# Kernel optimization log

Measured on AMD Instinct MI355X. Metric: run time of the kernel, lower is better.

The kernel has to match this reference:

```python
import jax, jax.numpy as jnp
import numpy as np

N_EMBED = 384
N_HEAD = 6
HEAD_SIZE = N_EMBED // N_HEAD  # 64
LN_EPS = 1e-5


def setup_inputs() -> dict:
    key = jax.random.key(0)
    ks = jax.random.split(key, 12)
    B, T = 128, 256
    s_in = 1.0 / np.sqrt(N_EMBED)
    s_ff = 1.0 / np.sqrt(4 * N_EMBED)
    return {
        "x": jax.random.normal(ks[0], (B, T, N_EMBED), jnp.float32),
        "Wq": jax.random.normal(ks[1], (N_HEAD, N_EMBED, HEAD_SIZE), jnp.float32) * s_in,
        "Wk": jax.random.normal(ks[2], (N_HEAD, N_EMBED, HEAD_SIZE), jnp.float32) * s_in,
        "Wv": jax.random.normal(ks[3], (N_HEAD, N_EMBED, HEAD_SIZE), jnp.float32) * s_in,
        "Wproj": jax.random.normal(ks[4], (N_EMBED, N_EMBED), jnp.float32) * s_in,
        "bproj": jnp.zeros((N_EMBED,), jnp.float32),
        "W1": jax.random.normal(ks[5], (N_EMBED, 4 * N_EMBED), jnp.float32) * s_in,
        "b1": jnp.zeros((4 * N_EMBED,), jnp.float32),
        "W2": jax.random.normal(ks[6], (4 * N_EMBED, N_EMBED), jnp.float32) * s_ff,
        "b2": jnp.zeros((N_EMBED,), jnp.float32),
        "ln1_g": jnp.ones((N_EMBED,), jnp.float32),
        "ln1_b": jnp.zeros((N_EMBED,), jnp.float32),
        "ln2_g": jnp.ones((N_EMBED,), jnp.float32),
        "ln2_b": jnp.zeros((N_EMBED,), jnp.float32),
    }


def _layernorm(x, g, b):
    mu = jnp.mean(x, axis=-1, keepdims=True)
    var = jnp.mean(jnp.square(x - mu), axis=-1, keepdims=True)
    return (x - mu) * jax.lax.rsqrt(var + LN_EPS) * g + b


def _attention(xn, Wq, Wk, Wv, Wproj, bproj):
    B, T, C = xn.shape
    q = jnp.einsum("btc,hcd->bhtd", xn, Wq)
    k = jnp.einsum("btc,hcd->bhtd", xn, Wk)
    v = jnp.einsum("btc,hcd->bhtd", xn, Wv)
    # NOTE: original scales by C**-0.5 with C = n_embed (384), not head_size
    scores = jnp.einsum("bhtd,bhsd->bhts", q, k) * (C ** -0.5)
    causal = jnp.tril(jnp.ones((T, T), bool))
    scores = jnp.where(causal, scores, -jnp.inf)
    wei = jax.nn.softmax(scores, axis=-1)
    out = jnp.einsum("bhts,bhsd->bhtd", wei, v)
    out = out.transpose(0, 2, 1, 3).reshape(B, T, N_EMBED)  # concat heads
    return out @ Wproj + bproj


def reference(x, Wq, Wk, Wv, Wproj, bproj, W1, b1, W2, b2, ln1_g, ln1_b, ln2_g, ln2_b):
    x = x + _attention(_layernorm(x, ln1_g, ln1_b), Wq, Wk, Wv, Wproj, bproj)
    h = _layernorm(x, ln2_g, ln2_b)
    ff = jax.nn.relu(h @ W1 + b1) @ W2 + b2
    return x + ff
```

## Files before the change

kernel.cpp:

```cpp
#include <hip/hip_runtime.h>
#include <hip/hip_bf16.h>

typedef __hip_bfloat16 bf16;
typedef __attribute__((ext_vector_type(8))) short bf16x8;
typedef __attribute__((ext_vector_type(4))) float f32x4;

#define CEMB 384
#define NHEAD 6
#define HSZ 64
#define TSEQ 256
#define BATCH 128
#define MROWS (BATCH*TSEQ)
#define FDIM 1536
#define QSCALE 0.05103103630798288f
#define SMAX 8.0f

#define AS1 __attribute__((address_space(1)))
#define AS3 __attribute__((address_space(3)))
__device__ __forceinline__ void gload16(const void* g, void* l){
  __builtin_amdgcn_global_load_lds((const AS1 unsigned*)(g), (AS3 unsigned*)(l), 16, 0, 0);
}
__device__ __forceinline__ float b2f(unsigned short u){
  unsigned int xi = ((unsigned int)u)<<16; float f; __builtin_memcpy(&f,&xi,4); return f;
}

__global__ __launch_bounds__(256) void ln_kernel(const float* __restrict__ x,
    const float* __restrict__ gam, const float* __restrict__ bet,
    bf16* __restrict__ y)
{
  const int row  = blockIdx.x*4 + (threadIdx.x>>6);
  const int lane = threadIdx.x & 63;
  const float* xr = x + (size_t)row*CEMB;
  float v[6]; float s = 0.f;
  #pragma unroll
  for (int i=0;i<6;i++){ v[i] = xr[lane + i*64]; s += v[i]; }
  #pragma unroll
  for (int m=1;m<64;m<<=1) s += __shfl_xor(s, m, 64);
  const float mu = s * (1.0f/CEMB);
  float qs = 0.f;
  #pragma unroll
  for (int i=0;i<6;i++){ v[i] -= mu; qs += v[i]*v[i]; }
  #pragma unroll
  for (int m=1;m<64;m<<=1) qs += __shfl_xor(qs, m, 64);
  const float rs = rsqrtf(qs*(1.0f/CEMB) + 1e-5f);
  bf16* yr = y + (size_t)row*CEMB;
  #pragma unroll
  for (int i=0;i<6;i++){
    int c = lane + i*64;
    yr[c] = __float2bfloat16(v[i]*rs*gam[c] + bet[c]);
  }
}

__global__ __launch_bounds__(256) void ln_kernel_b(const bf16* __restrict__ x,
    const float* __restrict__ gam, const float* __restrict__ bet,
    bf16* __restrict__ y)
{
  const int row  = blockIdx.x*4 + (threadIdx.x>>6);
  const int lane = threadIdx.x & 63;
  const ushort2* xr = (const ushort2*)(x + (size_t)row*CEMB);
  float v[6]; float s = 0.f;
  #pragma unroll
  for (int i=0;i<3;i++){
    ushort2 u = xr[lane + i*64];
    v[2*i]   = b2f(u.x); v[2*i+1] = b2f(u.y);
    s += v[2*i] + v[2*i+1];
  }
  #pragma unroll
  for (int m=1;m<64;m<<=1) s += __shfl_xor(s, m, 64);
  const float mu = s * (1.0f/CEMB);
  float qs = 0.f;
  #pragma unroll
  for (int i=0;i<6;i++){ v[i] -= mu; qs += v[i]*v[i]; }
  #pragma unroll
  for (int m=1;m<64;m<<=1) qs += __shfl_xor(qs, m, 64);
  const float rs = rsqrtf(qs*(1.0f/CEMB) + 1e-5f);
  bf16* yr = y + (size_t)row*CEMB;
  #pragma unroll
  for (int i=0;i<3;i++)
    #pragma unroll
    for (int j=0;j<2;j++){
      int c = (lane + i*64)*2 + j;
      yr[c] = __float2bfloat16(v[2*i+j]*rs*gam[c] + bet[c]);
    }
}

__global__ __launch_bounds__(256) void transpose_to_bf16(const float* __restrict__ src,
    bf16* __restrict__ dst, int K, int N)
{
  __shared__ float tile[32][33];
  const int n0 = blockIdx.x*32, k0 = blockIdx.y*32;
  src += (size_t)blockIdx.z*K*N;
  dst += (size_t)blockIdx.z*K*N;
  const int c = threadIdx.x & 31, r8 = threadIdx.x >> 5;
  #pragma unroll
  for (int i=0;i<4;i++)
    tile[r8 + i*8][c] = src[(size_t)(k0 + r8 + i*8)*N + n0 + c];
  __syncthreads();
  #pragma unroll
  for (int i=0;i<4;i++)
    dst[(size_t)(n0 + r8 + i*8)*K + k0 + c] = __float2bfloat16(tile[c][r8 + i*8]);
}

__global__ __launch_bounds__(256) void transpose_qkv(const float* __restrict__ Wq,
    const float* __restrict__ Wk, const float* __restrict__ Wv, bf16* __restrict__ dst)
{
  __shared__ float tile[32][33];
  const int z = blockIdx.z;
  const float* src = (z < 6) ? Wq : (z < 12 ? Wk : Wv);
  src += (size_t)(z % 6) * CEMB * HSZ;
  dst += (size_t)z * CEMB * HSZ;
  const int n0 = blockIdx.x*32, k0 = blockIdx.y*32;
  const int c = threadIdx.x & 31, r8 = threadIdx.x >> 5;
  #pragma unroll
  for (int i=0;i<4;i++)
    tile[r8 + i*8][c] = src[(size_t)(k0 + r8 + i*8)*HSZ + n0 + c];
  __syncthreads();
  #pragma unroll
  for (int i=0;i<4;i++)
    dst[(size_t)(n0 + r8 + i*8)*CEMB + k0 + c] = __float2bfloat16(tile[c][r8 + i*8]);
}

template<int EPI, int NN, int NK>
__global__ __launch_bounds__(512) void gemm5(
    const bf16* __restrict__ A, const bf16* __restrict__ BT,
    const float* __restrict__ bias, const float* __restrict__ resid,
    float* __restrict__ outf, bf16* __restrict__ outb0,
    bf16* __restrict__ outb1, bf16* __restrict__ outb2)
{
  constexpr int K = NK*32;
  constexpr int N = NN*128;
  __shared__ char lA[3][256*64];
  __shared__ char lB[3][128*64];
  const int cpx = gridDim.x >> 3;
  const int wg  = (blockIdx.x & 7)*cpx + (blockIdx.x >> 3);
  const int bm = (wg / NN)*256, bn = (wg % NN)*128;
  const int t = threadIdx.x, lane = t & 63, wid = t >> 6;
  const int wr = (wid>>1)*64, wc = (wid&1)*64;
  const int g = lane >> 4, fr = lane & 15;
  const size_t rowK2 = (size_t)K*2;
  f32x4 acc[4][4] = {};

  auto stage = [&](int sl, int kt){
    const size_t ko = (size_t)kt*64;
    #pragma unroll
    for (int i=0;i<2;i++){
      int slot = t + i*512;
      int row = slot>>2, blk = slot&3;
      gload16((const char*)A + (size_t)(bm+row)*rowK2 + ko + ((blk ^ ((row>>1)&3))<<4),
              lA[sl] + slot*16);
    }
    {
      int row = t>>2, blk = t&3;
      gload16((const char*)BT + (size_t)(bn+row)*rowK2 + ko + ((blk ^ ((row>>1)&3))<<4),
              lB[sl] + t*16);
    }
  };

  stage(0,0); stage(1,1); stage(2,2);
  #pragma unroll 1
  for (int kt=0; kt<NK; ++kt){
    const int rem = NK-1-kt;
    if (rem >= 2)      asm volatile("s_waitcnt vmcnt(6)" ::: "memory");
    else if (rem == 1) asm volatile("s_waitcnt vmcnt(3)" ::: "memory");
    else               asm volatile("s_waitcnt vmcnt(0)" ::: "memory");
    __builtin_amdgcn_s_barrier();
    const int cur = kt%3;
    bf16x8 af[4], bq[4];
    #pragma unroll
    for (int mi=0;mi<4;mi++){
      int row = wr + mi*16 + fr;
      af[mi] = *(const bf16x8*)(lA[cur] + row*64 + ((g ^ ((row>>1)&3))<<4));
    }
    #pragma unroll
    for (int nj=0;nj<4;nj++){
      int row = wc + nj*16 + fr;
      bq[nj] = *(const bf16x8*)(lB[cur] + row*64 + ((g ^ ((row>>1)&3))<<4));
    }
    asm volatile("s_waitcnt lgkmcnt(0)" ::: "memory");
    __builtin_amdgcn_sched_barrier(0);
    __builtin_amdgcn_s_barrier();
    if (kt+3 < NK) stage(cur, kt+3);
    __builtin_amdgcn_s_setprio(1);
    #pragma unroll
    for (int mi=0;mi<4;mi++)
      #pragma unroll
      for (int nj=0;nj<4;nj++)
        acc[mi][nj] = __builtin_amdgcn_mfma_f32_16x16x32_bf16(af[mi], bq[nj], acc[mi][nj], 0, 0, 0);
    __builtin_amdgcn_s_setprio(0);
  }

  if constexpr (EPI==0){
    const int sel = bn/CEMB;
    bf16* dst = sel==0 ? outb0 : (sel==1 ? outb1 : outb2);
    const float sc = sel==0 ? QSCALE : 1.0f;
    const int nb = bn - sel*CEMB;
    #pragma unroll
    for (int nj=0;nj<4;nj++){
      const int nn = nb + wc + nj*16 + fr;
      const int hh = nn>>6, dd = nn&63;
      #pragma unroll
      for (int mi=0;mi<4;mi++){
        const int m0 = bm + wr + mi*16 + 4*g;
        const int bb = m0>>8, tt0 = m0&255;
        bf16* p = dst + ((size_t)(bb*NHEAD + hh)*TSEQ + tt0)*HSZ + dd;
        #pragma unroll
        for (int e=0;e<4;e++)
          p[(size_t)e*HSZ] = __float2bfloat16(acc[mi][nj][e]*sc);
      }
    }
  } else {
    #pragma unroll
    for (int mi=0;mi<4;mi++)
      #pragma unroll
      for (int nj=0;nj<4;nj++)
        #pragma unroll
        for (int e=0;e<4;e++){
          const int m = bm + wr + mi*16 + 4*g + e;
          const int n = bn + wc + nj*16 + fr;
          const float vacc = acc[mi][nj][e];
          if constexpr (EPI==1){
            outb0[(size_t)m*N + n] = __float2bfloat16(vacc + bias[n] + resid[(size_t)m*N + n]);
          } else {
            float z = vacc + bias[n];
            outb0[(size_t)m*N + n] = __float2bfloat16(z > 0.f ? z : 0.f);
          }
        }
  }
}

template<int NK>
__global__ __launch_bounds__(512, 2) void gemm8n(
    const bf16* __restrict__ A, const bf16* __restrict__ BT,
    const float* __restrict__ bias, const bf16* __restrict__ residb,
    float* __restrict__ outf)
{
  constexpr int K = NK*64;
  __shared__ char lds[114688];
  const int cpx = gridDim.x >> 3;
  const int wg  = (blockIdx.x & 7)*cpx + (blockIdx.x >> 3);
  const int bm = (wg >> 1)*256, bn = (wg & 1)*192;
  const int t = threadIdx.x, lane = t & 63, wid = t >> 6;
  const int wm = wid >> 2, wn = wid & 3;
  const int g = lane >> 4, fr = lane & 15;
  const size_t rowb = (size_t)K*2;
  const int sblkA = ((t&3) ^ ((t>>3)&3)) << 4;
  const int swzA  = (g ^ ((fr>>1)&3)) << 4;
  f32x4 acc[8][3] = {};

  const char* Ag = (const char*)A + (size_t)(bm + (t>>2))*rowb + sblkA;
  const size_t rstep = rowb*128;

  auto stgA = [&](int KH, int sl, int kt2){
    const char* src = Ag + (size_t)kt2*128 + KH*64;
    char* dst = lds + sl*32768 + KH*16384 + wid*1024;
    gload16(src,         dst);
    gload16(src + rstep, dst + 8192);
  };
  auto stgB = [&](int sl, int kt2){
    #pragma unroll
    for (int j=0;j<3;j++){
      int slot = t + j*512;
      int row = slot>>3, blk = slot&7;
      gload16((const char*)BT + (size_t)(bn + row)*rowb + (size_t)kt2*128 + ((blk ^ (row&7))<<4),
              lds + 65536 + sl*24576 + j*8192 + wid*1024);
    }
  };
  auto rdA = [&](bf16x8* af, int sl, int MH, int KS){
    const char* p = lds + sl*32768 + KS*16384 + (wm*128 + MH*64 + fr)*64 + swzA;
    #pragma unroll
    for (int mi=0;mi<4;mi++) af[mi] = *(const bf16x8*)(p + mi*1024);
  };
  auto rdB = [&](bf16x8* bq, int sl, int ks){
    #pragma unroll
    for (int nj=0;nj<3;nj++){
      int row = wn*48 + nj*16 + fr;
      bq[nj] = *(const bf16x8*)(lds + 65536 + sl*24576 + row*128 + (((ks*4+g) ^ (row&7))<<4));
    }
  };

#define MFMA12(MH) \
  __builtin_amdgcn_s_setprio(1); \
  _Pragma("unroll") \
  for (int mi=0;mi<4;mi++){ \
    _Pragma("unroll") \
    for (int nj=0;nj<3;nj++) \
      acc[(MH)*4+mi][nj] = __builtin_amdgcn_mfma_f32_16x16x32_bf16(af[mi], bq[nj], acc[(MH)*4+mi][nj], 0, 0, 0); \
  } \
  __builtin_amdgcn_s_setprio(0);

  stgA(0,0,0); stgB(0,0); stgA(1,0,0);
  asm volatile("s_waitcnt vmcnt(2)" ::: "memory");
  __builtin_amdgcn_s_barrier();

  #pragma unroll 1
  for (int kt=0; kt<NK; ++kt){
    const int sl = kt&1, sn = sl^1;
    const bool pf = (kt+1 < NK);
    bf16x8 af[4], bq[3];
    rdA(af, sl, 0, 0); rdB(bq, sl, 0);
    if (pf) stgA(0,sn,kt+1);
    __builtin_amdgcn_s_barrier();
    asm volatile("s_waitcnt lgkmcnt(0)" ::: "memory");
    __builtin_amdgcn_sched_barrier(0);
    MFMA12(0)
    __builtin_amdgcn_s_barrier();
    rdA(af, sl, 1, 0);
    if (pf){ stgB(sn,kt+1);
             asm volatile("s_waitcnt vmcnt(5)" ::: "memory"); }
    else     asm volatile("s_waitcnt vmcnt(0)" ::: "memory");
    __builtin_amdgcn_s_barrier();
    asm volatile("s_waitcnt lgkmcnt(0)" ::: "memory");
    __builtin_amdgcn_sched_barrier(0);
    MFMA12(1)
    __builtin_amdgcn_s_barrier();
    rdA(af, sl, 0, 1); rdB(bq, sl, 1);
    if (pf) stgA(1,sn,kt+1);
    __builtin_amdgcn_s_barrier();
    asm volatile("s_waitcnt lgkmcnt(0)" ::: "memory");
    __builtin_amdgcn_sched_barrier(0);
    MFMA12(0)
    __builtin_amdgcn_s_barrier();
    rdA(af, sl, 1, 1);
    if (pf) asm volatile("s_waitcnt vmcnt(2)" ::: "memory");
    __builtin_amdgcn_s_barrier();
    asm volatile("s_waitcnt lgkmcnt(0)" ::: "memory");
    __builtin_amdgcn_sched_barrier(0);
    MFMA12(1)
    __builtin_amdgcn_s_barrier();
  }
#undef MFMA12

  #pragma unroll
  for (int mi=0;mi<8;mi++)
    #pragma unroll
    for (int nj=0;nj<3;nj++)
      #pragma unroll
      for (int e=0;e<4;e++){
        const int m = bm + wm*128 + mi*16 + 4*g + e;
        const int n = bn + wn*48 + nj*16 + fr;
        outf[(size_t)m*CEMB + n] = acc[mi][nj][e] + bias[n] +
            b2f(*(const unsigned short*)&residb[(size_t)m*CEMB + n]);
      }
}

__global__ __launch_bounds__(256) void attn_kernel(
    const bf16* __restrict__ q, const bf16* __restrict__ k,
    const bf16* __restrict__ v, bf16* __restrict__ out)
{
  __shared__ char kt_lds[64*128];
  __shared__ char vt_lds[80*128];
  __shared__ char p_lds[4][64*128];
  const int bh = blockIdx.x;
  const int bidx = bh / NHEAD, hidx = bh - bidx*NHEAD;
  const int t = threadIdx.x, lane = t & 63, w = t >> 6;
  const int g = lane >> 4, fr = lane & 15;
  const int lrow = lane >> 3;
  const int scol = ((lane & 7) ^ lrow) << 4;
  const size_t base = (size_t)bh * TSEQ * HSZ;

  if (t < 128){
    unsigned int ones2 = 0x3F803F80u;
    uint4 vv;
    if ((t>>3) == 0) vv = uint4{ones2, ones2, ones2, ones2};
    else             vv = uint4{0u, 0u, 0u, 0u};
    *(uint4*)(vt_lds + (64 + (t>>3))*128 + (t&7)*16) = vv;
  }

  bf16x8 qf[4][2];
  #pragma unroll
  for (int mi=0;mi<4;mi++)
    #pragma unroll
    for (int ks=0;ks<2;ks++)
      qf[mi][ks] = *(const bf16x8*)(q + base + (size_t)(w*64 + mi*16 + fr)*HSZ + ks*32 + g*8);

  f32x4 of[4][5] = {};

  for (int j=0;j<4;j++){
    __syncthreads();
    #pragma unroll
    for (int i=0;i<2;i++){
      int r0 = w*16 + i*8;
      gload16((const char*)(k + base + (size_t)(j*64 + r0 + lrow)*HSZ) + scol,
              kt_lds + r0*128);
    }
    #pragma unroll
    for (int i=0;i<2;i++){
      int chunk = t + i*256, r = chunk>>3, c = chunk&7;
      uint4 vv = *(const uint4*)(v + base + (size_t)(j*64 + r)*HSZ + c*8);
      const unsigned short* pv = (const unsigned short*)&vv;
      #pragma unroll
      for (int u=0;u<8;u++)
        *(unsigned short*)(vt_lds + (c*8+u)*128 + ((((r>>3) ^ u ^ c)&7)<<4) + (r&7)*2) = pv[u];
    }
    __syncthreads();
    if (j <= w){
      f32x4 sa[4][4] = {};
      #pragma unroll
      for (int ks=0;ks<2;ks++){
        bf16x8 kf[4];
        #pragma unroll
        for (int nj=0;nj<4;nj++)
          kf[nj] = *(const bf16x8*)(kt_lds + (nj*16+fr)*128 + (((ks*4+g)*16) ^ ((fr&7)<<4)));
        __builtin_amdgcn_s_setprio(1);
        #pragma unroll
        for (int mi=0;mi<4;mi++)
          #pragma unroll
          for (int nj=0;nj<4;nj++)
            sa[mi][nj] = __builtin_amdgcn_mfma_f32_16x16x32_bf16(qf[mi][ks], kf[nj], sa[mi][nj], 0, 0, 0);
        __builtin_amdgcn_s_setprio(0);
      }
      if (j == w){
        #pragma unroll
        for (int mi=0;mi<4;mi++)
          #pragma unroll
          for (int nj=0;nj<4;nj++)
            #pragma unroll
            for (int e=0;e<4;e++)
              if (nj*16 + fr > mi*16 + 4*g + e) sa[mi][nj][e] = -1e30f;
      }
      char* pl = p_lds[w];
      #pragma unroll
      for (int mi=0;mi<4;mi++)
        #pragma unroll
        for (int nj=0;nj<4;nj++)
          #pragma unroll
          for (int e=0;e<4;e++){
            int row = mi*16 + 4*g + e, col = nj*16 + fr;
            float p = __expf(sa[mi][nj][e] - SMAX);
            *(bf16*)(pl + row*128 + (((col>>3) ^ (row&7))<<4) + (col&7)*2) =
                __float2bfloat16(p);
          }
      #pragma unroll
      for (int ks=0;ks<2;ks++){
        bf16x8 pa[4], vf[5];
        #pragma unroll
        for (int mi=0;mi<4;mi++)
          pa[mi] = *(const bf16x8*)(pl + (mi*16+fr)*128 + (((ks*4+g)*16) ^ ((fr&7)<<4)));
        #pragma unroll
        for (int nd=0;nd<5;nd++){
          int d = nd*16 + fr;
          vf[nd] = *(const bf16x8*)(vt_lds + d*128 +
                   ((((ks*4+g) ^ (d&7) ^ ((d>>3)&7))&7)<<4));
        }
        __builtin_amdgcn_s_setprio(1);
        #pragma unroll
        for (int mi=0;mi<4;mi++)
          #pragma unroll
          for (int nd=0;nd<5;nd++)
            of[mi][nd] = __builtin_amdgcn_mfma_f32_16x16x32_bf16(pa[mi], vf[nd], of[mi][nd], 0, 0, 0);
        __builtin_amdgcn_s_setprio(0);
      }
    }
  }
  #pragma unroll
  for (int mi=0;mi<4;mi++){
    float rl[4];
    #pragma unroll
    for (int e=0;e<4;e++){
      float l = __shfl(of[mi][4][e], (int)(lane & 48), 64);
      rl[e] = 1.0f / l;
    }
    #pragma unroll
    for (int nd=0;nd<4;nd++)
      #pragma unroll
      for (int e=0;e<4;e++){
        int row = w*64 + mi*16 + 4*g + e;
        int d = nd*16 + fr;
        out[(size_t)(bidx*TSEQ + row)*CEMB + hidx*HSZ + d] =
            __float2bfloat16(of[mi][nd][e] * rl[e]);
      }
  }
}

extern "C" void kernel_launch(void* const* d_in, const int* in_sizes, int n_in,
                              void* d_out, int out_size, void* d_ws, size_t ws_size,
                              hipStream_t stream)
{
  const float* x     = (const float*)d_in[0];
  const float* Wq    = (const float*)d_in[1];
  const float* Wk    = (const float*)d_in[2];
  const float* Wv    = (const float*)d_in[3];
  const float* Wproj = (const float*)d_in[4];
  const float* bproj = (const float*)d_in[5];
  const float* W1    = (const float*)d_in[6];
  const float* b1    = (const float*)d_in[7];
  const float* W2    = (const float*)d_in[8];
  const float* b2    = (const float*)d_in[9];
  const float* ln1g  = (const float*)d_in[10];
  const float* ln1b  = (const float*)d_in[11];
  const float* ln2g  = (const float*)d_in[12];
  const float* ln2b  = (const float*)d_in[13];

  char* ws = (char*)d_ws;
  const size_t SA = (size_t)MROWS*CEMB*2;
  bf16* xn1    = (bf16*)(ws + 0*SA);
  bf16* qb     = (bf16*)(ws + 1*SA);
  bf16* kbuf   = (bf16*)(ws + 2*SA);
  bf16* vb     = (bf16*)(ws + 3*SA);
  bf16* attn_o = (bf16*)(ws + 0*SA);
  bf16* act    = (bf16*)(ws + 0*SA);
  bf16* hb     = (bf16*)(ws + 4*SA);
  bf16* x1b    = (bf16*)(ws + 5*SA);
  char* wb     = ws + 5*SA + (size_t)MROWS*CEMB*4;
  bf16* qkvT   = (bf16*)wb;
  bf16* projT  = (bf16*)(wb + (size_t)1152*384*2);
  bf16* w1T    = (bf16*)(wb + (size_t)(1152+384)*384*2);
  bf16* w2T    = (bf16*)(wb + (size_t)(1152+384+1536)*384*2);

  dim3 blk(256), blk5(512);
  transpose_qkv<<<dim3(2,12,18), blk, 0, stream>>>(Wq, Wk, Wv, qkvT);
  transpose_to_bf16<<<dim3(12,12,1), blk, 0, stream>>>(Wproj, projT, CEMB, CEMB);
  transpose_to_bf16<<<dim3(48,12,1), blk, 0, stream>>>(W1,    w1T,   CEMB, FDIM);
  transpose_to_bf16<<<dim3(12,48,1), blk, 0, stream>>>(W2,    w2T,   FDIM, CEMB);

  ln_kernel<<<dim3(MROWS/4), blk, 0, stream>>>(x, ln1g, ln1b, xn1);
  gemm5<0,9,12><<<dim3(1152), blk5, 0, stream>>>(xn1, qkvT, nullptr, nullptr,
                                                 nullptr, qb, kbuf, vb);
  attn_kernel<<<dim3(768), blk, 0, stream>>>(qb, kbuf, vb, attn_o);
  gemm5<1,3,12><<<dim3(384), blk5, 0, stream>>>(attn_o, projT, bproj, x,
                                                nullptr, x1b, nullptr, nullptr);
  ln_kernel_b<<<dim3(MROWS/4), blk, 0, stream>>>(x1b, ln2g, ln2b, hb);
  gemm5<2,12,12><<<dim3(1536), blk5, 0, stream>>>(hb, w1T, b1, nullptr,
                                                  nullptr, act, nullptr, nullptr);
  gemm8n<24><<<dim3(256), blk5, 0, stream>>>(act, w2T, b2, x1b, (float*)d_out);
}
```

Before: 248.4 us.

## Replace gemm5 with 256x192-tile gemm8e using 8-wave ping-pong pipeline

Replaces the 256x128-tile triple-buffered GEMM used for QKV, projection and FFN1 with a 256x192-tile kernel that streams K in 64-wide chunks through double-buffered LDS. Each wave now owns a 128x48 output slab with 24 accumulators, and loads are interleaved with four MFMA phases per K step. The goal is more data reuse per tile, fewer workgroups, and better overlap of global-to-LDS copies with MFMA work. The cost is more accumulator registers and more barriers per iteration, and launch bounds of (512,2) may limit occupancy or cause spills.

```diff
diff --git a/kernel.cpp b/kernel.cpp
--- a/kernel.cpp
+++ b/kernel.cpp
@@ -120,74 +120,108 @@
     dst[(size_t)(n0 + r8 + i*8)*CEMB + k0 + c] = __float2bfloat16(tile[c][r8 + i*8]);
 }
 
-template<int EPI, int NN, int NK>
-__global__ __launch_bounds__(512) void gemm5(
+template<int EPI, int NT>
+__global__ __launch_bounds__(512, 2) void gemm8e(
     const bf16* __restrict__ A, const bf16* __restrict__ BT,
-    const float* __restrict__ bias, const float* __restrict__ resid,
-    float* __restrict__ outf, bf16* __restrict__ outb0,
-    bf16* __restrict__ outb1, bf16* __restrict__ outb2)
-{
-  constexpr int K = NK*32;
-  constexpr int N = NN*128;
-  __shared__ char lA[3][256*64];
-  __shared__ char lB[3][128*64];
+    const float* __restrict__ bias, const float* __restrict__ residf,
+    bf16* __restrict__ outb0, bf16* __restrict__ outb1, bf16* __restrict__ outb2)
+{
+  constexpr int K = 384, NK = 6;
+  constexpr int N = NT*192;
+  __shared__ char lds[114688];
   const int cpx = gridDim.x >> 3;
   const int wg  = (blockIdx.x & 7)*cpx + (blockIdx.x >> 3);
-  const int bm = (wg / NN)*256, bn = (wg % NN)*128;
+  const int bm = (wg / NT)*256, bn = (wg % NT)*192;
   const int t = threadIdx.x, lane = t & 63, wid = t >> 6;
-  const int wr = (wid>>1)*64, wc = (wid&1)*64;
+  const int wm = wid >> 2, wn = wid & 3;
   const int g = lane >> 4, fr = lane & 15;
-  const size_t rowK2 = (size_t)K*2;
-  f32x4 acc[4][4] = {};
-
-  auto stage = [&](int sl, int kt){
-    const size_t ko = (size_t)kt*64;
-    #pragma unroll
-    for (int i=0;i<2;i++){
-      int slot = t + i*512;
-      int row = slot>>2, blk = slot&3;
-      gload16((const char*)A + (size_t)(bm+row)*rowK2 + ko + ((blk ^ ((row>>1)&3))<<4),
-              lA[sl] + slot*16);
-    }
-    {
-      int row = t>>2, blk = t&3;
-      gload16((const char*)BT + (size_t)(bn+row)*rowK2 + ko + ((blk ^ ((row>>1)&3))<<4),
-              lB[sl] + t*16);
-    }
-  };
-
-  stage(0,0); stage(1,1); stage(2,2);
+  const size_t rowb = (size_t)K*2;
+  const int sblkA = ((t&3) ^ ((t>>3)&3)) << 4;
+  const int swzA  = (g ^ ((fr>>1)&3)) << 4;
+  f32x4 acc[8][3] = {};
+
+  const char* Ag = (const char*)A + (size_t)(bm + (t>>2))*rowb + sblkA;
+  const size_t rstep = rowb*128;
+
+  auto stgA = [&](int KH, int sl, int kt2){
+    const char* src = Ag + (size_t)kt2*128 + KH*64;
+    char* dst = lds + sl*32768 + KH*16384 + wid*1024;
+    gload16(src,         dst);
+    gload16(src + rstep, dst + 8192);
+  };
+  auto stgB = [&](int sl, int kt2){
+    #pragma unroll
+    for (int j=0;j<3;j++){
+      int slot = t + j*512;
+      int row = slot>>3, blk = slot&7;
+      gload16((const char*)BT + (size_t)(bn + row)*rowb + (size_t)kt2*128 + ((blk ^ (row&7))<<4),
+              lds + 65536 + sl*24576 + j*8192 + wid*1024);
+    }
+  };
+  auto rdA = [&](bf16x8* af, int sl, int MH, int KS){
+    const char* p = lds + sl*32768 + KS*16384 + (wm*128 + MH*64 + fr)*64 + swzA;
+    #pragma unroll
+    for (int mi=0;mi<4;mi++) af[mi] = *(const bf16x8*)(p + mi*1024);
+  };
+  auto rdB = [&](bf16x8* bq, int sl, int ks){
+    #pragma unroll
+    for (int nj=0;nj<3;nj++){
+      int row = wn*48 + nj*16 + fr;
+      bq[nj] = *(const bf16x8*)(lds + 65536 + sl*24576 + row*128 + (((ks*4+g) ^ (row&7))<<4));
+    }
+  };
+
+#define MFMA12(MH) \
+  __builtin_amdgcn_s_setprio(1); \
+  _Pragma("unroll") \
+  for (int mi=0;mi<4;mi++){ \
+    _Pragma("unroll") \
+    for (int nj=0;nj<3;nj++) \
+      acc[(MH)*4+mi][nj] = __builtin_amdgcn_mfma_f32_16x16x32_bf16(af[mi], bq[nj], acc[(MH)*4+mi][nj], 0, 0, 0); \
+  } \
+  __builtin_amdgcn_s_setprio(0);
+
+  stgA(0,0,0); stgB(0,0); stgA(1,0,0);
+  asm volatile("s_waitcnt vmcnt(2)" ::: "memory");
+  __builtin_amdgcn_s_barrier();
+
   #pragma unroll 1
   for (int kt=0; kt<NK; ++kt){
-    const int rem = NK-1-kt;
-    if (rem >= 2)      asm volatile("s_waitcnt vmcnt(6)" ::: "memory");
-    else if (rem == 1) asm volatile("s_waitcnt vmcnt(3)" ::: "memory");
-    else               asm volatile("s_waitcnt vmcnt(0)" ::: "memory");
-    __builtin_amdgcn_s_barrier();
-    const int cur = kt%3;
-    bf16x8 af[4], bq[4];
-    #pragma unroll
-    for (int mi=0;mi<4;mi++){
-      int row = wr + mi*16 + fr;
-      af[mi] = *(const bf16x8*)(lA[cur] + row*64 + ((g ^ ((row>>1)&3))<<4));
-    }
-    #pragma unroll
-    for (int nj=0;nj<4;nj++){
-      int row = wc + nj*16 + fr;
-      bq[nj] = *(const bf16x8*)(lB[cur] + row*64 + ((g ^ ((row>>1)&3))<<4));
-    }
-    asm volatile("s_waitcnt lgkmcnt(0)" ::: "memory");
-    __builtin_amdgcn_sched_barrier(0);
-    __builtin_amdgcn_s_barrier();
-    if (kt+3 < NK) stage(cur, kt+3);
-    __builtin_amdgcn_s_setprio(1);
-    #pragma unroll
-    for (int mi=0;mi<4;mi++)
-      #pragma unroll
-      for (int nj=0;nj<4;nj++)
-        acc[mi][nj] = __builtin_amdgcn_mfma_f32_16x16x32_bf16(af[mi], bq[nj], acc[mi][nj], 0, 0, 0);
-    __builtin_amdgcn_s_setprio(0);
-  }
+    const int sl = kt&1, sn = sl^1;
+    const bool pf = (kt+1 < NK);
+    bf16x8 af[4], bq[3];
+    rdA(af, sl, 0, 0); rdB(bq, sl, 0);
+    if (pf) stgA(0,sn,kt+1);
+    __builtin_amdgcn_s_barrier();
+    asm volatile("s_waitcnt lgkmcnt(0)" ::: "memory");
+    __builtin_amdgcn_sched_barrier(0);
+    MFMA12(0)
+    __builtin_amdgcn_s_barrier();
+    rdA(af, sl, 1, 0);
+    if (pf){ stgB(sn,kt+1);
+             asm volatile("s_waitcnt vmcnt(5)" ::: "memory"); }
+    else     asm volatile("s_waitcnt vmcnt(0)" ::: "memory");
+    __builtin_amdgcn_s_barrier();
+    asm volatile("s_waitcnt lgkmcnt(0)" ::: "memory");
+    __builtin_amdgcn_sched_barrier(0);
+    MFMA12(1)
+    __builtin_amdgcn_s_barrier();
+    rdA(af, sl, 0, 1); rdB(bq, sl, 1);
+    if (pf) stgA(1,sn,kt+1);
+    __builtin_amdgcn_s_barrier();
+    asm volatile("s_waitcnt lgkmcnt(0)" ::: "memory");
+    __builtin_amdgcn_sched_barrier(0);
+    MFMA12(0)
+    __builtin_amdgcn_s_barrier();
+    rdA(af, sl, 1, 1);
+    if (pf) asm volatile("s_waitcnt vmcnt(2)" ::: "memory");
+    __builtin_amdgcn_s_barrier();
+    asm volatile("s_waitcnt lgkmcnt(0)" ::: "memory");
+    __builtin_amdgcn_sched_barrier(0);
+    MFMA12(1)
+    __builtin_amdgcn_s_barrier();
+  }
+#undef MFMA12
 
   if constexpr (EPI==0){
     const int sel = bn/CEMB;
@@ -195,12 +229,12 @@
     const float sc = sel==0 ? QSCALE : 1.0f;
     const int nb = bn - sel*CEMB;
     #pragma unroll
-    for (int nj=0;nj<4;nj++){
-      const int nn = nb + wc + nj*16 + fr;
+    for (int nj=0;nj<3;nj++){
+      const int nn = nb + wn*48 + nj*16 + fr;
       const int hh = nn>>6, dd = nn&63;
       #pragma unroll
-      for (int mi=0;mi<4;mi++){
-        const int m0 = bm + wr + mi*16 + 4*g;
+      for (int mi=0;mi<8;mi++){
+        const int m0 = bm + wm*128 + mi*16 + 4*g;
         const int bb = m0>>8, tt0 = m0&255;
         bf16* p = dst + ((size_t)(bb*NHEAD + hh)*TSEQ + tt0)*HSZ + dd;
         #pragma unroll
@@ -210,16 +244,16 @@
     }
   } else {
     #pragma unroll
-    for (int mi=0;mi<4;mi++)
-      #pragma unroll
-      for (int nj=0;nj<4;nj++)
+    for (int mi=0;mi<8;mi++)
+      #pragma unroll
+      for (int nj=0;nj<3;nj++)
         #pragma unroll
         for (int e=0;e<4;e++){
-          const int m = bm + wr + mi*16 + 4*g + e;
-          const int n = bn + wc + nj*16 + fr;
+          const int m = bm + wm*128 + mi*16 + 4*g + e;
+          const int n = bn + wn*48 + nj*16 + fr;
           const float vacc = acc[mi][nj][e];
           if constexpr (EPI==1){
-            outb0[(size_t)m*N + n] = __float2bfloat16(vacc + bias[n] + resid[(size_t)m*N + n]);
+            outb0[(size_t)m*N + n] = __float2bfloat16(vacc + bias[n] + residf[(size_t)m*N + n]);
           } else {
             float z = vacc + bias[n];
             outb0[(size_t)m*N + n] = __float2bfloat16(z > 0.f ? z : 0.f);
@@ -514,13 +548,13 @@
   transpose_to_bf16<<<dim3(12,48,1), blk, 0, stream>>>(W2,    w2T,   FDIM, CEMB);
 
   ln_kernel<<<dim3(MROWS/4), blk, 0, stream>>>(x, ln1g, ln1b, xn1);
-  gemm5<0,9,12><<<dim3(1152), blk5, 0, stream>>>(xn1, qkvT, nullptr, nullptr,
-                                                 nullptr, qb, kbuf, vb);
+  gemm8e<0,6><<<dim3(768), blk5, 0, stream>>>(xn1, qkvT, nullptr, nullptr,
+                                              qb, kbuf, vb);
   attn_kernel<<<dim3(768), blk, 0, stream>>>(qb, kbuf, vb, attn_o);
-  gemm5<1,3,12><<<dim3(384), blk5, 0, stream>>>(attn_o, projT, bproj, x,
-                                                nullptr, x1b, nullptr, nullptr);
+  gemm8e<1,2><<<dim3(256), blk5, 0, stream>>>(attn_o, projT, bproj, x,
+                                              x1b, nullptr, nullptr);
   ln_kernel_b<<<dim3(MROWS/4), blk, 0, stream>>>(x1b, ln2g, ln2b, hb);
-  gemm5<2,12,12><<<dim3(1536), blk5, 0, stream>>>(hb, w1T, b1, nullptr,
-                                                  nullptr, act, nullptr, nullptr);
+  gemm8e<2,8><<<dim3(1024), blk5, 0, stream>>>(hb, w1T, b1, nullptr,
+                                               act, nullptr, nullptr);
   gemm8n<24><<<dim3(256), blk5, 0, stream>>>(act, w2T, b2, x1b, (float*)d_out);
 }
```

New measurement: 255.3 us. 1.03x slower.

## Interleave query rows across waves to balance causal attention work

Applied to the files above, without the earlier changes.

Each wave used to own a contiguous 64-row query block, so under the causal mask wave 0 did one KV tile while wave 3 did four. The change gives each wave four 16-row strips, one from each 64-row block, so every wave does the same amount of work per KV tile. The P scratch buffer shrinks to 16 rows per wave and the j loop is fully unrolled. Each wave now issues smaller MFMA batches with more serial dependence per strip, which lowers the instruction-level parallelism inside a wave.

```diff
diff --git a/kernel.cpp b/kernel.cpp
--- a/kernel.cpp
+++ b/kernel.cpp
@@ -349,7 +349,7 @@
 {
   __shared__ char kt_lds[64*128];
   __shared__ char vt_lds[80*128];
-  __shared__ char p_lds[4][64*128];
+  __shared__ char p_lds[4][16*128];
   const int bh = blockIdx.x;
   const int bidx = bh / NHEAD, hidx = bh - bidx*NHEAD;
   const int t = threadIdx.x, lane = t & 63, w = t >> 6;
@@ -368,13 +368,14 @@
 
   bf16x8 qf[4][2];
   #pragma unroll
-  for (int mi=0;mi<4;mi++)
+  for (int s=0;s<4;s++)
     #pragma unroll
     for (int ks=0;ks<2;ks++)
-      qf[mi][ks] = *(const bf16x8*)(q + base + (size_t)(w*64 + mi*16 + fr)*HSZ + ks*32 + g*8);
+      qf[s][ks] = *(const bf16x8*)(q + base + (size_t)(s*64 + w*16 + fr)*HSZ + ks*32 + g*8);
 
   f32x4 of[4][5] = {};
 
+  #pragma unroll
   for (int j=0;j<4;j++){
     __syncthreads();
     #pragma unroll
@@ -393,8 +394,10 @@
         *(unsigned short*)(vt_lds + (c*8+u)*128 + ((((r>>3) ^ u ^ c)&7)<<4) + (r&7)*2) = pv[u];
     }
     __syncthreads();
-    if (j <= w){
-      f32x4 sa[4][4] = {};
+    #pragma unroll
+    for (int s=0;s<4;s++){
+      if (s < j) continue;
+      f32x4 sa[4] = {};
       #pragma unroll
       for (int ks=0;ks<2;ks++){
         bf16x8 kf[4];
@@ -403,39 +406,31 @@
           kf[nj] = *(const bf16x8*)(kt_lds + (nj*16+fr)*128 + (((ks*4+g)*16) ^ ((fr&7)<<4)));
         __builtin_amdgcn_s_setprio(1);
         #pragma unroll
-        for (int mi=0;mi<4;mi++)
-          #pragma unroll
-          for (int nj=0;nj<4;nj++)
-            sa[mi][nj] = __builtin_amdgcn_mfma_f32_16x16x32_bf16(qf[mi][ks], kf[nj], sa[mi][nj], 0, 0, 0);
+        for (int nj=0;nj<4;nj++)
+          sa[nj] = __builtin_amdgcn_mfma_f32_16x16x32_bf16(qf[s][ks], kf[nj], sa[nj], 0, 0, 0);
         __builtin_amdgcn_s_setprio(0);
       }
-      if (j == w){
-        #pragma unroll
-        for (int mi=0;mi<4;mi++)
+      if (s == j){
+        #pragma unroll
+        for (int nj=0;nj<4;nj++)
           #pragma unroll
-          for (int nj=0;nj<4;nj++)
-            #pragma unroll
-            for (int e=0;e<4;e++)
-              if (nj*16 + fr > mi*16 + 4*g + e) sa[mi][nj][e] = -1e30f;
+          for (int e=0;e<4;e++)
+            if (nj*16 + fr > w*16 + 4*g + e) sa[nj][e] = -1e30f;
       }
       char* pl = p_lds[w];
       #pragma unroll
-      for (int mi=0;mi<4;mi++)
-        #pragma unroll
-        for (int nj=0;nj<4;nj++)
-          #pragma unroll
-          for (int e=0;e<4;e++){
-            int row = mi*16 + 4*g + e, col = nj*16 + fr;
-            float p = __expf(sa[mi][nj][e] - SMAX);
-            *(bf16*)(pl + row*128 + (((col>>3) ^ (row&7))<<4) + (col&7)*2) =
-                __float2bfloat16(p);
-          }
+      for (int nj=0;nj<4;nj++)
+        #pragma unroll
+        for (int e=0;e<4;e++){
+          int row16 = 4*g + e, col = nj*16 + fr;
+          float p = __expf(sa[nj][e] - SMAX);
+          *(bf16*)(pl + row16*128 + (((col>>3) ^ (row16&7))<<4) + (col&7)*2) =
+              __float2bfloat16(p);
+        }
       #pragma unroll
       for (int ks=0;ks<2;ks++){
-        bf16x8 pa[4], vf[5];
-        #pragma unroll
-        for (int mi=0;mi<4;mi++)
-          pa[mi] = *(const bf16x8*)(pl + (mi*16+fr)*128 + (((ks*4+g)*16) ^ ((fr&7)<<4)));
+        bf16x8 pa, vf[5];
+        pa = *(const bf16x8*)(pl + fr*128 + (((ks*4+g)*16) ^ ((fr&7)<<4)));
         #pragma unroll
         for (int nd=0;nd<5;nd++){
           int d = nd*16 + fr;
@@ -444,30 +439,28 @@
         }
         __builtin_amdgcn_s_setprio(1);
         #pragma unroll
-        for (int mi=0;mi<4;mi++)
-          #pragma unroll
-          for (int nd=0;nd<5;nd++)
-            of[mi][nd] = __builtin_amdgcn_mfma_f32_16x16x32_bf16(pa[mi], vf[nd], of[mi][nd], 0, 0, 0);
+        for (int nd=0;nd<5;nd++)
+          of[s][nd] = __builtin_amdgcn_mfma_f32_16x16x32_bf16(pa, vf[nd], of[s][nd], 0, 0, 0);
         __builtin_amdgcn_s_setprio(0);
       }
     }
   }
   #pragma unroll
-  for (int mi=0;mi<4;mi++){
+  for (int s=0;s<4;s++){
     float rl[4];
     #pragma unroll
     for (int e=0;e<4;e++){
-      float l = __shfl(of[mi][4][e], (int)(lane & 48), 64);
+      float l = __shfl(of[s][4][e], (int)(lane & 48), 64);
       rl[e] = 1.0f / l;
     }
     #pragma unroll
     for (int nd=0;nd<4;nd++)
       #pragma unroll
       for (int e=0;e<4;e++){
-        int row = w*64 + mi*16 + 4*g + e;
+        int row = s*64 + w*16 + 4*g + e;
         int d = nd*16 + fr;
         out[(size_t)(bidx*TSEQ + row)*CEMB + hidx*HSZ + d] =
-            __float2bfloat16(of[mi][nd][e] * rl[e]);
+            __float2bfloat16(of[s][nd][e] * rl[e]);
       }
   }
 }
```

Result: faster. 236.7 us (-4.7%).
